# Kernel tuning notes

Hardware: AMD Instinct MI355X
Metric: run time of the kernel (lower is better)

## Reference

```python
import jax, jax.numpy as jnp
import numpy as np

B, L, F, R = 32, 128, 128, 4096
MAX_INTERIOR = R >> 1  # tpr.max_interior_index
N = 262144


def setup_inputs() -> dict:
    key = jax.random.key(0)
    ks = jax.random.split(key, 7)
    mem_values = jax.random.normal(ks[0], (N, F), dtype=jnp.float32)
    # zero out a slice of rows so the ConsNet pad_mask path is exercised
    mem_values = mem_values.at[: N // 20].set(0.0)
    arg_weights = jax.random.uniform(ks[1], (B, L, 4), dtype=jnp.float32)
    root_filler = jax.random.normal(ks[2], (B, F), dtype=jnp.float32)
    op_dist = jax.random.uniform(ks[3], (B, 3), dtype=jnp.float32)
    batch_idx = jax.random.randint(ks[4], (N,), 0, B, dtype=jnp.int32)
    slot_idx = jax.random.randint(ks[5], (N,), 0, L, dtype=jnp.int32)
    role_idx = jax.random.randint(ks[6], (N,), 0, R, dtype=jnp.int32)
    return {
        "mem_values": mem_values,
        "arg_weights": arg_weights,
        "root_filler": root_filler,
        "op_dist": op_dist,
        "batch_idx": batch_idx,
        "slot_idx": slot_idx,
        "role_idx": role_idx,
    }


def _forward(mem_values, arg_weights, root_filler, op_dist,
             batch_idx, slot_idx, role_idx):
    # per-entry gather of the 4 argument weights: w[n,k] = arg_weights[b_n, l_n, k]
    w = arg_weights[batch_idx, slot_idx]  # [N, 4]
    flat = batch_idx.astype(jnp.int32) * R + role_idx  # [N], coalesce key (b, r)

    def coalesce(vals):  # scatter-add == torch_sparse.coalesce into dense [B,R,F]
        g = jnp.zeros((B * R, F), vals.dtype).at[flat].add(vals)
        return g.reshape(B, R, F)

    H = R >> 1

    # ---- CarNet (sparse): weight, coalesce, keep even roles, role >>= 1 ----
    car_A = coalesce(mem_values * w[:, 0:1])            # [B,R,F]
    car_out = jnp.zeros((B, R, F), mem_values.dtype).at[:, :H].set(car_A[:, 0::2])

    # ---- CdrNet (sparse): keep odd roles != 1, role >>= 1 ----
    cdr_A = coalesce(mem_values * w[:, 1:2])
    cdr_half = cdr_A[:, 1::2]                            # roles 2r+1 -> r
    cdr_half = cdr_half.at[:, 0].set(0.0)                # exclude old role 1 (r=0)
    cdr_out = jnp.zeros((B, R, F), mem_values.dtype).at[:, :H].set(cdr_half)

    # ---- ConsNet (sparse): pad-mask weights, roles<MAX_INTERIOR, children + root ----
    pad = jnp.all(mem_values == 0, axis=1, keepdims=True)  # [N,1]
    c1 = coalesce(mem_values * jnp.where(pad, 0.0, w[:, 2:3]))
    c2 = coalesce(mem_values * jnp.where(pad, 0.0, w[:, 3:4]))
    cons_out = jnp.zeros((B, R, F), mem_values.dtype)
    cons_out = cons_out.at[:, 0::2].set(c1[:, :MAX_INTERIOR])      # r -> 2r
    cons_out = cons_out.at[:, 1::2].add(c2[:, :MAX_INTERIOR])      # r -> 2r+1
    cons_out = cons_out.at[:, 1].add(root_filler)                  # root at role 1

    # ---- op-distribution weighted combine (coalesce of the 3 streams) ----
    out = (op_dist[:, 0, None, None] * car_out
           + op_dist[:, 1, None, None] * cdr_out
           + op_dist[:, 2, None, None] * cons_out)
    return out


def reference(mem_values, arg_weights, root_filler, op_dist,
              batch_idx, slot_idx, role_idx):
    return _forward(mem_values, arg_weights, root_filler, op_dist,
                    batch_idx, slot_idx, role_idx)
```

## Files before the change

### kernel.cpp

```cpp
#include <hip/hip_runtime.h>


namespace {
constexpr int kB = 32;
constexpr int kL = 128;
constexpr int kF = 128;
constexpr int kR = 4096;
constexpr int kN = 262144;
constexpr int kNB = kB * kR;
constexpr int kCapMax = 32;
constexpr int kOvfMax = 65536;

constexpr size_t kOffCounts  = 0;
constexpr size_t kOffOvfCnt  = 524288;
constexpr size_t kOffOvf     = 524304;
constexpr size_t kOffEntries = 1572880;
}

__global__ __launch_bounds__(256) void build_kernel(
    const float4* __restrict__ aw, const float* __restrict__ opd,
    const int* __restrict__ bidx, const int* __restrict__ sidx,
    const int* __restrict__ ridx, int cap,
    int* __restrict__ counts, int* __restrict__ ovf_cnt,
    int4* __restrict__ ovf, int2* __restrict__ entries) {
  int n = blockIdx.x * 256 + threadIdx.x;
  if (n >= kN) return;
  int b = bidx[n];
  int s = sidx[n];
  int rr = ridx[n];
  float4 w = aw[b * kL + s];
  float op0 = opd[3 * b + 0];
  float op1 = opd[3 * b + 1];
  float op2 = opd[3 * b + 2];
  const int base = b << 12;

  auto push = [&](int row, float sc) {
    int key = base | row;
    int pos = atomicAdd(&counts[key], 1);
    if (pos < cap) {
      entries[(size_t)key * cap + pos] = make_int2(n, __float_as_int(sc));
    } else {
      int o = atomicAdd(ovf_cnt, 1);
      if (o < kOvfMax) ovf[o] = make_int4(key, n, __float_as_int(sc), 0);
    }
  };

  if ((rr & 1) == 0) {
    push(rr >> 1, op0 * w.x);
  } else if (rr >= 3) {
    push((rr - 1) >> 1, op1 * w.y);
  }
  if (rr < kR / 2) {
    push(2 * rr, op2 * w.z);
    push(2 * rr + 1, op2 * w.w);
  }
}

__device__ __forceinline__ void proc4(int i0, int cnt, int2 e,
                                      const float2* __restrict__ mem2, int t,
                                      float& ax, float& ay) {
  int n0 = __builtin_amdgcn_readfirstlane(__shfl(e.x, i0 + 0));
  int s0 = __builtin_amdgcn_readfirstlane(__shfl(e.y, i0 + 0));
  int n1 = __builtin_amdgcn_readfirstlane(__shfl(e.x, i0 + 1));
  int s1 = __builtin_amdgcn_readfirstlane(__shfl(e.y, i0 + 1));
  int n2 = __builtin_amdgcn_readfirstlane(__shfl(e.x, i0 + 2));
  int s2 = __builtin_amdgcn_readfirstlane(__shfl(e.y, i0 + 2));
  int n3 = __builtin_amdgcn_readfirstlane(__shfl(e.x, i0 + 3));
  int s3 = __builtin_amdgcn_readfirstlane(__shfl(e.y, i0 + 3));
  const bool v1 = (i0 + 1) < cnt, v2 = (i0 + 2) < cnt, v3 = (i0 + 3) < cnt;
  n1 = v1 ? n1 : 0;
  n2 = v2 ? n2 : 0;
  n3 = v3 ? n3 : 0;
  float f0 = __int_as_float(s0);
  float f1 = v1 ? __int_as_float(s1) : 0.f;
  float f2 = v2 ? __int_as_float(s2) : 0.f;
  float f3 = v3 ? __int_as_float(s3) : 0.f;
  float2 m0 = mem2[(size_t)n0 * (kF / 2) + t];
  float2 m1 = mem2[(size_t)n1 * (kF / 2) + t];
  float2 m2 = mem2[(size_t)n2 * (kF / 2) + t];
  float2 m3 = mem2[(size_t)n3 * (kF / 2) + t];
  ax += f0 * m0.x; ay += f0 * m0.y;
  ax += f1 * m1.x; ay += f1 * m1.y;
  ax += f2 * m2.x; ay += f2 * m2.y;
  ax += f3 * m3.x; ay += f3 * m3.y;
}

__global__ __launch_bounds__(256) void gather_kernel(
    const float2* __restrict__ mem2, const float2* __restrict__ root2,
    const float* __restrict__ opd, const int* __restrict__ counts,
    const int2* __restrict__ entries, int cap, float2* __restrict__ out2) {
  const int row = blockIdx.x * 4 + (threadIdx.x >> 6);
  const int t = threadIdx.x & 63;
  int cnt = min(counts[row], cap);
  cnt = __builtin_amdgcn_readfirstlane(cnt);

  float ax = 0.f, ay = 0.f;
  if (cnt > 0) {
    int2 e = make_int2(0, 0);
    if (t < cnt) e = entries[(size_t)row * cap + t];
    for (int i = 0; i < cnt; i += 4) proc4(i, cnt, e, mem2, t, ax, ay);
  }

  const int r = row & (kR - 1);
  if (r == 1) {
    const int b = row >> 12;
    float op2 = opd[3 * b + 2];
    float2 rf = root2[b * (kF / 2) + t];
    ax += op2 * rf.x;
    ay += op2 * rf.y;
  }
  float2 o;
  o.x = ax;
  o.y = ay;
  out2[(size_t)row * (kF / 2) + t] = o;
}

__global__ __launch_bounds__(128) void ovf_kernel(
    const float* __restrict__ mem, const int* __restrict__ ovf_cnt,
    const int4* __restrict__ ovf, float* __restrict__ out) {
  int m = *ovf_cnt;
  if (m > kOvfMax) m = kOvfMax;
  const int t = threadIdx.x;
  for (int i = blockIdx.x; i < m; i += gridDim.x) {
    int4 e = ovf[i];
    float sc = __int_as_float(e.z);
    atomicAdd(&out[(size_t)e.x * kF + t], sc * mem[(size_t)e.y * kF + t]);
  }
}

extern "C" void kernel_launch(void* const* d_in, const int* in_sizes, int n_in,
                              void* d_out, int out_size, void* d_ws, size_t ws_size,
                              hipStream_t stream) {
  const float* mem   = (const float*)d_in[0];
  const float* aw    = (const float*)d_in[1];
  const float* rootf = (const float*)d_in[2];
  const float* opd   = (const float*)d_in[3];
  const int* bidx    = (const int*)d_in[4];
  const int* sidx    = (const int*)d_in[5];
  const int* ridx    = (const int*)d_in[6];

  char* ws = (char*)d_ws;
  int* counts    = (int*)(ws + kOffCounts);
  int* ovf_cnt   = (int*)(ws + kOffOvfCnt);
  int4* ovf      = (int4*)(ws + kOffOvf);
  int2* entries  = (int2*)(ws + kOffEntries);

  int cap = kCapMax;
  if (ws_size > kOffEntries) {
    size_t avail = (ws_size - kOffEntries) / ((size_t)kNB * sizeof(int2));
    if (avail < (size_t)cap) cap = (int)avail;
  } else {
    cap = 0;
  }

  hipMemsetAsync(ws, 0, kOffOvfCnt + 4, stream);

  build_kernel<<<kN / 256, 256, 0, stream>>>(
      (const float4*)aw, opd, bidx, sidx, ridx, cap, counts, ovf_cnt, ovf,
      entries);

  gather_kernel<<<kNB / 4, 256, 0, stream>>>(
      (const float2*)mem, (const float2*)rootf, opd, counts, entries, cap,
      (float2*)d_out);

  ovf_kernel<<<64, 128, 0, stream>>>(mem, ovf_cnt, ovf, (float*)d_out);
}
```

Measured before the change: 299.5 us.

## Pair output rows so cons entries share one memory load across two rows

```diff
diff --git a/kernel.cpp b/kernel.cpp
--- a/kernel.cpp
+++ b/kernel.cpp
@@ -7,22 +7,26 @@
 constexpr int kF = 128;
 constexpr int kR = 4096;
 constexpr int kN = 262144;
-constexpr int kNB = kB * kR;
-constexpr int kCapMax = 32;
+constexpr int kQ = 2048;
+constexpr int kNP = kB * kQ;
+constexpr int kCap = 16;
 constexpr int kOvfMax = 65536;
 
-constexpr size_t kOffCounts  = 0;
+constexpr size_t kOffRowCnt  = 0;
+constexpr size_t kOffConsCnt = 262144;
 constexpr size_t kOffOvfCnt  = 524288;
 constexpr size_t kOffOvf     = 524304;
-constexpr size_t kOffEntries = 1572880;
+constexpr size_t kOffRowEnt  = 1572880;
+constexpr size_t kOffConsEnt = 9961488;
 }
 
 __global__ __launch_bounds__(256) void build_kernel(
     const float4* __restrict__ aw, const float* __restrict__ opd,
     const int* __restrict__ bidx, const int* __restrict__ sidx,
-    const int* __restrict__ ridx, int cap,
-    int* __restrict__ counts, int* __restrict__ ovf_cnt,
-    int4* __restrict__ ovf, int2* __restrict__ entries) {
+    const int* __restrict__ ridx,
+    int* __restrict__ rowcnt, int* __restrict__ conscnt,
+    int* __restrict__ ovf_cnt, int4* __restrict__ ovf,
+    int2* __restrict__ rowent, int4* __restrict__ consent) {
   int n = blockIdx.x * 256 + threadIdx.x;
   if (n >= kN) return;
   int b = bidx[n];
@@ -32,87 +36,216 @@
   float op0 = opd[3 * b + 0];
   float op1 = opd[3 * b + 1];
   float op2 = opd[3 * b + 2];
-  const int base = b << 12;
-
-  auto push = [&](int row, float sc) {
-    int key = base | row;
-    int pos = atomicAdd(&counts[key], 1);
-    if (pos < cap) {
-      entries[(size_t)key * cap + pos] = make_int2(n, __float_as_int(sc));
+
+  bool even = (rr & 1) == 0;
+  if (even || rr >= 3) {
+    float sc = even ? op0 * w.x : op1 * w.y;
+    int key = (b << 11) | (rr >> 1);
+    int pos = atomicAdd(&rowcnt[key], 1);
+    if (pos < kCap) {
+      rowent[key * kCap + pos] = make_int2(n, __float_as_int(sc));
     } else {
       int o = atomicAdd(ovf_cnt, 1);
-      if (o < kOvfMax) ovf[o] = make_int4(key, n, __float_as_int(sc), 0);
-    }
-  };
-
-  if ((rr & 1) == 0) {
-    push(rr >> 1, op0 * w.x);
-  } else if (rr >= 3) {
-    push((rr - 1) >> 1, op1 * w.y);
-  }
-  if (rr < kR / 2) {
-    push(2 * rr, op2 * w.z);
-    push(2 * rr + 1, op2 * w.w);
-  }
-}
-
-__device__ __forceinline__ void proc4(int i0, int cnt, int2 e,
-                                      const float2* __restrict__ mem2, int t,
-                                      float& ax, float& ay) {
-  int n0 = __builtin_amdgcn_readfirstlane(__shfl(e.x, i0 + 0));
-  int s0 = __builtin_amdgcn_readfirstlane(__shfl(e.y, i0 + 0));
-  int n1 = __builtin_amdgcn_readfirstlane(__shfl(e.x, i0 + 1));
-  int s1 = __builtin_amdgcn_readfirstlane(__shfl(e.y, i0 + 1));
-  int n2 = __builtin_amdgcn_readfirstlane(__shfl(e.x, i0 + 2));
-  int s2 = __builtin_amdgcn_readfirstlane(__shfl(e.y, i0 + 2));
-  int n3 = __builtin_amdgcn_readfirstlane(__shfl(e.x, i0 + 3));
-  int s3 = __builtin_amdgcn_readfirstlane(__shfl(e.y, i0 + 3));
-  const bool v1 = (i0 + 1) < cnt, v2 = (i0 + 2) < cnt, v3 = (i0 + 3) < cnt;
-  n1 = v1 ? n1 : 0;
-  n2 = v2 ? n2 : 0;
-  n3 = v3 ? n3 : 0;
-  float f0 = __int_as_float(s0);
-  float f1 = v1 ? __int_as_float(s1) : 0.f;
-  float f2 = v2 ? __int_as_float(s2) : 0.f;
-  float f3 = v3 ? __int_as_float(s3) : 0.f;
-  float2 m0 = mem2[(size_t)n0 * (kF / 2) + t];
-  float2 m1 = mem2[(size_t)n1 * (kF / 2) + t];
-  float2 m2 = mem2[(size_t)n2 * (kF / 2) + t];
-  float2 m3 = mem2[(size_t)n3 * (kF / 2) + t];
-  ax += f0 * m0.x; ay += f0 * m0.y;
-  ax += f1 * m1.x; ay += f1 * m1.y;
-  ax += f2 * m2.x; ay += f2 * m2.y;
-  ax += f3 * m3.x; ay += f3 * m3.y;
+      if (o < kOvfMax)
+        ovf[o] = make_int4(b * kR + (rr >> 1), n, __float_as_int(sc), 0);
+    }
+  }
+  if (rr < kQ) {
+    int key = (b << 11) | rr;
+    int pos = atomicAdd(&conscnt[key], 1);
+    if (pos < kCap) {
+      consent[key * kCap + pos] =
+          make_int4(n, __float_as_int(op2 * w.z), __float_as_int(op2 * w.w), 0);
+    } else {
+      int o = atomicAdd(ovf_cnt, 2);
+      if (o < kOvfMax)
+        ovf[o] = make_int4(b * kR + 2 * rr, n, __float_as_int(op2 * w.z), 0);
+      if (o + 1 < kOvfMax)
+        ovf[o + 1] =
+            make_int4(b * kR + 2 * rr + 1, n, __float_as_int(op2 * w.w), 0);
+    }
+  }
 }
 
 __global__ __launch_bounds__(256) void gather_kernel(
     const float2* __restrict__ mem2, const float2* __restrict__ root2,
-    const float* __restrict__ opd, const int* __restrict__ counts,
-    const int2* __restrict__ entries, int cap, float2* __restrict__ out2) {
-  const int row = blockIdx.x * 4 + (threadIdx.x >> 6);
+    const float* __restrict__ opd,
+    const int* __restrict__ rowcnt, const int* __restrict__ conscnt,
+    const int2* __restrict__ rowent, const int2* __restrict__ consent2,
+    float2* __restrict__ out2) {
+  const int p = blockIdx.x * 4 + (threadIdx.x >> 6);
   const int t = threadIdx.x & 63;
-  int cnt = min(counts[row], cap);
-  cnt = __builtin_amdgcn_readfirstlane(cnt);
-
-  float ax = 0.f, ay = 0.f;
-  if (cnt > 0) {
-    int2 e = make_int2(0, 0);
-    if (t < cnt) e = entries[(size_t)row * cap + t];
-    for (int i = 0; i < cnt; i += 4) proc4(i, cnt, e, mem2, t, ax, ay);
-  }
-
-  const int r = row & (kR - 1);
-  if (r == 1) {
-    const int b = row >> 12;
+  const int b = p >> 11;
+  const int q = p & (kQ - 1);
+  const bool hashalf = q < 1024;
+
+  int cn_raw = conscnt[p];
+  int2 ce = make_int2(0, 0);
+  if (t < 32) ce = (consent2 + (size_t)p * 2 * kCap)[t];
+  int2 hc = make_int2(0, 0);
+  int2 he = make_int2(0, 0);
+  if (hashalf) {
+    int key0 = (b << 11) | (q << 1);
+    hc = *(const int2*)(rowcnt + key0);
+    if (t < 32) he = (rowent + (size_t)key0 * kCap)[t];
+  }
+  int cn = min(__builtin_amdgcn_readfirstlane(cn_raw), kCap);
+  int h0 = 0, h1 = 0;
+  if (hashalf) {
+    h0 = min(__builtin_amdgcn_readfirstlane(hc.x), kCap);
+    h1 = min(__builtin_amdgcn_readfirstlane(hc.y), kCap);
+  }
+
+  float2 mc[4];
+  float c1s[4], c2s[4];
+#pragma unroll
+  for (int j = 0; j < 4; ++j) {
+    c1s[j] = 0.f;
+    c2s[j] = 0.f;
+    mc[j] = make_float2(0.f, 0.f);
+  }
+  if (cn > 0) {
+#pragma unroll
+    for (int j = 0; j < 4; ++j) {
+      bool v = j < cn;
+      int nn = __shfl(ce.x, 2 * j);
+      float a = __int_as_float(__shfl(ce.y, 2 * j));
+      float bb = __int_as_float(__shfl(ce.x, 2 * j + 1));
+      nn = v ? nn : 0;
+      c1s[j] = v ? a : 0.f;
+      c2s[j] = v ? bb : 0.f;
+      mc[j] = mem2[(size_t)nn * (kF / 2) + t];
+    }
+  }
+  float2 m0[8], m1[8];
+  float s0a[8], s1a[8];
+#pragma unroll
+  for (int j = 0; j < 8; ++j) {
+    s0a[j] = 0.f;
+    s1a[j] = 0.f;
+    m0[j] = make_float2(0.f, 0.f);
+    m1[j] = make_float2(0.f, 0.f);
+  }
+  if (h0 > 0) {
+#pragma unroll
+    for (int j = 0; j < 4; ++j) {
+      bool v = j < h0;
+      int nn = __shfl(he.x, j);
+      float s = __int_as_float(__shfl(he.y, j));
+      nn = v ? nn : 0;
+      s0a[j] = v ? s : 0.f;
+      m0[j] = mem2[(size_t)nn * (kF / 2) + t];
+    }
+    if (h0 > 4) {
+#pragma unroll
+      for (int j = 4; j < 8; ++j) {
+        bool v = j < h0;
+        int nn = __shfl(he.x, j);
+        float s = __int_as_float(__shfl(he.y, j));
+        nn = v ? nn : 0;
+        s0a[j] = v ? s : 0.f;
+        m0[j] = mem2[(size_t)nn * (kF / 2) + t];
+      }
+    }
+  }
+  if (h1 > 0) {
+#pragma unroll
+    for (int j = 0; j < 4; ++j) {
+      bool v = j < h1;
+      int nn = __shfl(he.x, 16 + j);
+      float s = __int_as_float(__shfl(he.y, 16 + j));
+      nn = v ? nn : 0;
+      s1a[j] = v ? s : 0.f;
+      m1[j] = mem2[(size_t)nn * (kF / 2) + t];
+    }
+    if (h1 > 4) {
+#pragma unroll
+      for (int j = 4; j < 8; ++j) {
+        bool v = j < h1;
+        int nn = __shfl(he.x, 16 + j);
+        float s = __int_as_float(__shfl(he.y, 16 + j));
+        nn = v ? nn : 0;
+        s1a[j] = v ? s : 0.f;
+        m1[j] = mem2[(size_t)nn * (kF / 2) + t];
+      }
+    }
+  }
+
+  float ax0 = 0.f, ay0 = 0.f, ax1 = 0.f, ay1 = 0.f;
+#pragma unroll
+  for (int j = 0; j < 4; ++j) {
+    ax0 += c1s[j] * mc[j].x;
+    ay0 += c1s[j] * mc[j].y;
+    ax1 += c2s[j] * mc[j].x;
+    ay1 += c2s[j] * mc[j].y;
+  }
+#pragma unroll
+  for (int j = 0; j < 8; ++j) {
+    ax0 += s0a[j] * m0[j].x;
+    ay0 += s0a[j] * m0[j].y;
+  }
+#pragma unroll
+  for (int j = 0; j < 8; ++j) {
+    ax1 += s1a[j] * m1[j].x;
+    ay1 += s1a[j] * m1[j].y;
+  }
+
+  for (int i = 4; i < cn; i += 4) {
+#pragma unroll
+    for (int j = 0; j < 4; ++j) {
+      int idx = i + j;
+      bool v = idx < cn;
+      int nn = __shfl(ce.x, 2 * idx);
+      float a = __int_as_float(__shfl(ce.y, 2 * idx));
+      float bb = __int_as_float(__shfl(ce.x, 2 * idx + 1));
+      nn = v ? nn : 0;
+      a = v ? a : 0.f;
+      bb = v ? bb : 0.f;
+      float2 m = mem2[(size_t)nn * (kF / 2) + t];
+      ax0 += a * m.x;
+      ay0 += a * m.y;
+      ax1 += bb * m.x;
+      ay1 += bb * m.y;
+    }
+  }
+  for (int i = 8; i < h0; i += 4) {
+#pragma unroll
+    for (int j = 0; j < 4; ++j) {
+      int idx = i + j;
+      bool v = idx < h0;
+      int nn = __shfl(he.x, idx);
+      float s = __int_as_float(__shfl(he.y, idx));
+      nn = v ? nn : 0;
+      s = v ? s : 0.f;
+      float2 m = mem2[(size_t)nn * (kF / 2) + t];
+      ax0 += s * m.x;
+      ay0 += s * m.y;
+    }
+  }
+  for (int i = 8; i < h1; i += 4) {
+#pragma unroll
+    for (int j = 0; j < 4; ++j) {
+      int idx = i + j;
+      bool v = idx < h1;
+      int nn = __shfl(he.x, 16 + idx);
+      float s = __int_as_float(__shfl(he.y, 16 + idx));
+      nn = v ? nn : 0;
+      s = v ? s : 0.f;
+      float2 m = mem2[(size_t)nn * (kF / 2) + t];
+      ax1 += s * m.x;
+      ay1 += s * m.y;
+    }
+  }
+
+  if (q == 0) {
     float op2 = opd[3 * b + 2];
     float2 rf = root2[b * (kF / 2) + t];
-    ax += op2 * rf.x;
-    ay += op2 * rf.y;
-  }
-  float2 o;
-  o.x = ax;
-  o.y = ay;
-  out2[(size_t)row * (kF / 2) + t] = o;
+    ax1 += op2 * rf.x;
+    ay1 += op2 * rf.y;
+  }
+  size_t orow = ((size_t)b * kR + 2 * q) * (kF / 2) + t;
+  out2[orow] = make_float2(ax0, ay0);
+  out2[orow + (kF / 2)] = make_float2(ax1, ay1);
 }
 
 __global__ __launch_bounds__(128) void ovf_kernel(
@@ -140,28 +273,22 @@
   const int* ridx    = (const int*)d_in[6];
 
   char* ws = (char*)d_ws;
-  int* counts    = (int*)(ws + kOffCounts);
-  int* ovf_cnt   = (int*)(ws + kOffOvfCnt);
-  int4* ovf      = (int4*)(ws + kOffOvf);
-  int2* entries  = (int2*)(ws + kOffEntries);
-
-  int cap = kCapMax;
-  if (ws_size > kOffEntries) {
-    size_t avail = (ws_size - kOffEntries) / ((size_t)kNB * sizeof(int2));
-    if (avail < (size_t)cap) cap = (int)avail;
-  } else {
-    cap = 0;
-  }
-
-  hipMemsetAsync(ws, 0, kOffOvfCnt + 4, stream);
+  int* rowcnt   = (int*)(ws + kOffRowCnt);
+  int* conscnt  = (int*)(ws + kOffConsCnt);
+  int* ovf_cnt  = (int*)(ws + kOffOvfCnt);
+  int4* ovf     = (int4*)(ws + kOffOvf);
+  int2* rowent  = (int2*)(ws + kOffRowEnt);
+  int4* consent = (int4*)(ws + kOffConsEnt);
+
+  hipMemsetAsync(ws, 0, kOffOvfCnt + 16, stream);
 
   build_kernel<<<kN / 256, 256, 0, stream>>>(
-      (const float4*)aw, opd, bidx, sidx, ridx, cap, counts, ovf_cnt, ovf,
-      entries);
-
-  gather_kernel<<<kNB / 4, 256, 0, stream>>>(
-      (const float2*)mem, (const float2*)rootf, opd, counts, entries, cap,
-      (float2*)d_out);
+      (const float4*)aw, opd, bidx, sidx, ridx, rowcnt, conscnt, ovf_cnt, ovf,
+      rowent, consent);
+
+  gather_kernel<<<kNP / 4, 256, 0, stream>>>(
+      (const float2*)mem, (const float2*)rootf, opd, rowcnt, conscnt, rowent,
+      (const int2*)consent, (float2*)d_out);
 
   ovf_kernel<<<64, 128, 0, stream>>>(mem, ovf_cnt, ovf, (float*)d_out);
 }
```

Result: faster. 265.3 us (-11.4%).
